# Kernel optimization log

Measured on AMD Instinct MI355X. Metric: run time of the kernel, lower is better.

## Reference

```python
import jax, jax.numpy as jnp
import numpy as np

N = 50000   # num_nodes
D = 128     # h_dim
R = 32      # num_rels * 2 (forward + inverse relations)
B = 8       # num_bases
E = 600000  # num_edges


def setup_inputs() -> dict:
    key = jax.random.key(0)
    ks = jax.random.split(key, 14)
    s = 1.0 / np.sqrt(D)
    return {
        "h_ids": jnp.arange(N, dtype=jnp.int32),
        "src": jax.random.randint(ks[0], (E,), 0, N),
        "dst": jax.random.randint(ks[1], (E,), 0, N),
        "etype": jax.random.randint(ks[2], (E,), 0, R),
        "norm": jax.random.uniform(ks[3], (E, 1), dtype=jnp.float32),
        "embedding": jax.random.normal(ks[4], (N, D), dtype=jnp.float32) * 0.05,
        "w_comp1": jax.random.normal(ks[5], (R, B), dtype=jnp.float32) * (1.0 / np.sqrt(B)),
        "bases1": jax.random.normal(ks[6], (B, D, D), dtype=jnp.float32) * s,
        "loop_w1": jax.random.normal(ks[7], (D, D), dtype=jnp.float32) * s,
        "bias1": jnp.zeros((D,), dtype=jnp.float32),
        "w_comp2": jax.random.normal(ks[8], (R, B), dtype=jnp.float32) * (1.0 / np.sqrt(B)),
        "bases2": jax.random.normal(ks[9], (B, D, D), dtype=jnp.float32) * s,
        "loop_w2": jax.random.normal(ks[10], (D, D), dtype=jnp.float32) * s,
        "bias2": jnp.zeros((D,), dtype=jnp.float32),
    }


def _rel_graph_conv(h, src, dst, etype, norm, w_comp, bases, loop_w, bias, act):
    # basis decomposition: W[r] = sum_b w_comp[r,b] * bases[b]
    W = jnp.einsum('rb,bio->rio', w_comp, bases)          # [R, D, D]
    # transform every node by every relation weight (dense GEMM)
    all_t = jnp.einsum('ni,rio->nro', h, W)               # [N, R, D]
    # per-edge gather of relation-specific transformed source features
    msg = all_t[src, etype] * norm                        # [E, D]
    # scatter-aggregate messages at destination nodes
    agg = jax.ops.segment_sum(msg, dst, num_segments=h.shape[0])  # [N, D]
    out = agg + h @ loop_w + bias                         # self-loop + bias
    return act(out) if act is not None else out


def reference(h_ids, src, dst, etype, norm, embedding,
              w_comp1, bases1, loop_w1, bias1,
              w_comp2, bases2, loop_w2, bias2):
    # EmbeddingLayer
    h = embedding[h_ids]                                  # [N, D]
    # hidden layer 0: relu activation (idx < num_hidden_layers-1)
    h = _rel_graph_conv(h, src, dst, etype, norm, w_comp1, bases1, loop_w1, bias1, jax.nn.relu)
    # hidden layer 1: no activation (last layer)
    h = _rel_graph_conv(h, src, dst, etype, norm, w_comp2, bases2, loop_w2, bias2, None)
    return h
```

## Files before the change

kernel.cpp:

```cpp
#include <hip/hip_runtime.h>

#define DD 128
#define NB 8
#define KTOT 1152

typedef unsigned int uint_t;
typedef __attribute__((ext_vector_type(8))) _Float16 half8v;
typedef __attribute__((ext_vector_type(2))) _Float16 half2v;
typedef __attribute__((ext_vector_type(4))) float f32x4;

static __device__ __forceinline__ void gld_lds16(const _Float16* g, _Float16* l)
{
  __builtin_amdgcn_global_load_lds(
      (const __attribute__((address_space(1))) void*)g,
      (__attribute__((address_space(3))) void*)l, 16, 0, 0);
}

static __device__ __forceinline__ half2v bc_h2(uint_t u)
{
  union { uint_t u; half2v h; } c; c.u = u; return c.h;
}

static __device__ __forceinline__ float fdot2(uint_t a, uint_t b, float acc)
{
#if __has_builtin(__builtin_amdgcn_fdot2)
  return __builtin_amdgcn_fdot2(bc_h2(a), bc_h2(b), acc, false);
#else
  half2v x = bc_h2(a), y = bc_h2(b);
  return acc + (float)x[0] * (float)y[0] + (float)x[1] * (float)y[1];
#endif
}

__global__ __launch_bounds__(256) void k_prep_w(
    const float* __restrict__ bases1, const float* __restrict__ loopw1,
    const float* __restrict__ bases2, const float* __restrict__ loopw2,
    _Float16* __restrict__ WcA)
{
  int i = blockIdx.x * 256 + threadIdx.x;
  if (i >= 2 * 36 * DD * 32) return;
  int layer = i / (36 * DD * 32);
  int rem   = i % (36 * DD * 32);
  int ks    = rem / (DD * 32);
  int rem2  = rem % (DD * 32);
  int feat  = rem2 / 32;
  int j     = rem2 % 32;
  int k     = ks * 32 + j;
  const float* basesL = layer ? bases2 : bases1;
  const float* loopwL = layer ? loopw2 : loopw1;
  float v;
  if (k < 1024) {
    int kk = k >> 3, b = k & 7;
    v = basesL[((size_t)b * DD + kk) * DD + feat];
  } else {
    v = loopwL[(size_t)(k - 1024) * DD + feat];
  }
  WcA[i] = (_Float16)v;
}

__global__ __launch_bounds__(256) void k_cast(
    const float* __restrict__ h, const int* __restrict__ ids,
    _Float16* __restrict__ hf, int N)
{
  int i = blockIdx.x * 256 + threadIdx.x;
  if (i >= N * (DD / 8)) return;
  int n  = i / (DD / 8);
  int k8 = (i % (DD / 8)) * 8;
  int row = ids ? ids[n] : n;
  const float* hp = h + (size_t)row * DD + k8;
  float4 v0 = *(const float4*)hp;
  float4 v1 = *(const float4*)(hp + 4);
  union { _Float16 e[8]; uint4 q; } p;
  p.e[0]=(_Float16)v0.x; p.e[1]=(_Float16)v0.y; p.e[2]=(_Float16)v0.z; p.e[3]=(_Float16)v0.w;
  p.e[4]=(_Float16)v1.x; p.e[5]=(_Float16)v1.y; p.e[6]=(_Float16)v1.z; p.e[7]=(_Float16)v1.w;
  *(uint4*)&hf[(size_t)n * DD + k8] = p.q;
}

__global__ __launch_bounds__(256) void k_zero(int* __restrict__ p, int n)
{
  int i = blockIdx.x * 256 + threadIdx.x;
  if (i < n) p[i] = 0;
}

__global__ __launch_bounds__(256) void k_hist(
    const int* __restrict__ dst, int* __restrict__ cnt, int E)
{
  int e = blockIdx.x * 256 + threadIdx.x;
  if (e < E) atomicAdd(&cnt[dst[e]], 1);
}

__global__ __launch_bounds__(256) void k_bsum(
    const int* __restrict__ cnt, int* __restrict__ bsum, int N)
{
  __shared__ int s[256];
  int i = blockIdx.x * 256 + threadIdx.x;
  s[threadIdx.x] = (i < N) ? ((cnt[i] + 1) & ~1) : 0;
  __syncthreads();
  for (int off = 128; off > 0; off >>= 1) {
    if (threadIdx.x < off) s[threadIdx.x] += s[threadIdx.x + off];
    __syncthreads();
  }
  if (threadIdx.x == 0) bsum[blockIdx.x] = s[0];
}

__global__ __launch_bounds__(256) void k_scanb(
    const int* __restrict__ bsum, int* __restrict__ boff, int nb)
{
  __shared__ int s[256];
  int t = threadIdx.x;
  int own = (t < nb) ? bsum[t] : 0;
  s[t] = own;
  __syncthreads();
  for (int off = 1; off < 256; off <<= 1) {
    int v = (t >= off) ? s[t - off] : 0;
    __syncthreads();
    s[t] += v;
    __syncthreads();
  }
  if (t < nb) boff[t] = s[t] - own;
}

__global__ __launch_bounds__(256) void k_scan3(
    const int* __restrict__ cnt, const int* __restrict__ boff,
    int* __restrict__ row_start, int N)
{
  __shared__ int s[256];
  int t = threadIdx.x;
  int i = blockIdx.x * 256 + t;
  int v = (i < N) ? ((cnt[i] + 1) & ~1) : 0;
  s[t] = v;
  __syncthreads();
  for (int off = 1; off < 256; off <<= 1) {
    int u = (t >= off) ? s[t - off] : 0;
    __syncthreads();
    s[t] += u;
    __syncthreads();
  }
  if (i < N) row_start[i] = boff[blockIdx.x] + s[t] - v;
}

__global__ __launch_bounds__(256) void k_pad(
    const int* __restrict__ rowst, const int* __restrict__ cnt,
    int* __restrict__ psrc, int N)
{
  int v = blockIdx.x * 256 + threadIdx.x;
  if (v < N && (cnt[v] & 1)) {
    int slot = rowst[v] + cnt[v];
    psrc[slot] = 0;
  }
}

__global__ __launch_bounds__(256) void k_place(
    const int* __restrict__ dst, const int* __restrict__ src,
    const int* __restrict__ etype, const float* __restrict__ norm,
    const int* __restrict__ row_start, int* __restrict__ cursor,
    int* __restrict__ psrc, int2* __restrict__ en, int E)
{
  int e = blockIdx.x * 256 + threadIdx.x;
  if (e < E) {
    int v = dst[e];
    int slot = row_start[v] + atomicAdd(&cursor[v], 1);
    psrc[slot] = src[e];
    en[slot] = make_int2(etype[e], __float_as_int(norm[e]));
  }
}

__global__ __launch_bounds__(256) void k_payload_pair(
    const int2* __restrict__ en,
    const float* __restrict__ wcomp1, const float* __restrict__ wcomp2,
    _Float16* __restrict__ c1, _Float16* __restrict__ c2, int npair)
{
  int i = blockIdx.x * 256 + threadIdx.x;
  if (i >= npair) return;
  int2 e0 = en[2 * i], e1 = en[2 * i + 1];
  float n0 = __int_as_float(e0.y), n1 = __int_as_float(e1.y);
  const float* w10 = wcomp1 + e0.x * NB;
  const float* w11 = wcomp1 + e1.x * NB;
  const float* w20 = wcomp2 + e0.x * NB;
  const float* w21 = wcomp2 + e1.x * NB;

  union { _Float16 h[16]; uint4 q[2]; } p;
  #pragma unroll
  for (int b = 0; b < NB; b++) {
    p.h[b * 2]     = (_Float16)(w10[b] * n0);
    p.h[b * 2 + 1] = (_Float16)(w11[b] * n1);
  }
  *(uint4*)&c1[(size_t)i * 16]     = p.q[0];
  *(uint4*)&c1[(size_t)i * 16 + 8] = p.q[1];
  #pragma unroll
  for (int b = 0; b < NB; b++) {
    p.h[b * 2]     = (_Float16)(w20[b] * n0);
    p.h[b * 2 + 1] = (_Float16)(w21[b] * n1);
  }
  *(uint4*)&c2[(size_t)i * 16]     = p.q[0];
  *(uint4*)&c2[(size_t)i * 16 + 8] = p.q[1];
}

__global__ __launch_bounds__(256) void k_agg(
    const int* __restrict__ rowst, const int* __restrict__ cnt,
    const int* __restrict__ psrc, const _Float16* __restrict__ cpair,
    const _Float16* __restrict__ hf,
    _Float16* __restrict__ agg, int N)
{
  int v = blockIdx.x * 4 + (threadIdx.x >> 6);
  if (v >= N) return;
  int lane = threadIdx.x & 63;
  const uint_t* hf32 = (const uint_t*)hf;
  const int beg = rowst[v];
  const int npairs = (cnt[v] + 1) >> 1;
  const uint_t* cp = (const uint_t*)cpair + (size_t)(beg >> 1) * 8;
  const int* ps = psrc + beg;

  float ax[NB] = {}, ay[NB] = {};
  int i = 0;
  for (; i + 2 <= npairs; i += 2) {
    int s0 = ps[2*i + 0], s1 = ps[2*i + 1];
    int s2 = ps[2*i + 2], s3 = ps[2*i + 3];
    uint_t u0 = hf32[(size_t)s0 * 64 + lane];
    uint_t u1 = hf32[(size_t)s1 * 64 + lane];
    uint_t u2 = hf32[(size_t)s2 * 64 + lane];
    uint_t u3 = hf32[(size_t)s3 * 64 + lane];
    uint_t lo01 = __builtin_amdgcn_perm(u0, u1, 0x01000504);
    uint_t hi01 = __builtin_amdgcn_perm(u0, u1, 0x03020706);
    uint_t lo23 = __builtin_amdgcn_perm(u2, u3, 0x01000504);
    uint_t hi23 = __builtin_amdgcn_perm(u2, u3, 0x03020706);
    #pragma unroll
    for (int b = 0; b < NB; b++) {
      uint_t ca = cp[(size_t)i * 8 + b];
      uint_t cb = cp[(size_t)(i + 1) * 8 + b];
      ax[b] = fdot2(ca, lo01, ax[b]);
      ay[b] = fdot2(ca, hi01, ay[b]);
      ax[b] = fdot2(cb, lo23, ax[b]);
      ay[b] = fdot2(cb, hi23, ay[b]);
    }
  }
  if (i < npairs) {
    int s0 = ps[2*i + 0], s1 = ps[2*i + 1];
    uint_t u0 = hf32[(size_t)s0 * 64 + lane];
    uint_t u1 = hf32[(size_t)s1 * 64 + lane];
    uint_t lo01 = __builtin_amdgcn_perm(u0, u1, 0x01000504);
    uint_t hi01 = __builtin_amdgcn_perm(u0, u1, 0x03020706);
    #pragma unroll
    for (int b = 0; b < NB; b++) {
      uint_t ca = cp[(size_t)i * 8 + b];
      ax[b] = fdot2(ca, lo01, ax[b]);
      ay[b] = fdot2(ca, hi01, ay[b]);
    }
  }

  union { _Float16 e[8]; uint4 q; } p0, p1;
  #pragma unroll
  for (int b = 0; b < NB; b++) { p0.e[b] = (_Float16)ax[b]; p1.e[b] = (_Float16)ay[b]; }
  uint4* dstp = (uint4*)&agg[(size_t)v * 1024 + lane * 16];
  dstp[0] = p0.q;
  dstp[1] = p1.q;
}

template <int LAYER>
__global__ __launch_bounds__(256) void k_mm(
    const _Float16* __restrict__ agg,
    const _Float16* __restrict__ hf,
    const _Float16* __restrict__ WcA,
    const float* __restrict__ bias,
    float* __restrict__ outf, _Float16* __restrict__ outh, int N)
{
  __shared__ _Float16 sB[2][2048];

  const int n0   = blockIdx.x * 32;
  const int wv   = threadIdx.x >> 6;
  const int lane = threadIdx.x & 63;
  const int l15  = lane & 15, l4 = lane >> 4;

  int nodeS = n0 + (lane & 31); if (nodeS >= N) nodeS = N - 1;
  const int ksl = 2 * wv + (lane >> 5);

  f32x4 acc[2][2];
  #pragma unroll
  for (int a = 0; a < 2; a++)
    #pragma unroll
    for (int b = 0; b < 2; b++) acc[a][b] = (f32x4)0.f;

  const int fbase = wv * 32 + l15;
  const int koff  = l4 * 8;

  auto STAGE = [&](int buf, int t) {
    const _Float16* g;
    if (t < 16) g = &agg[(size_t)nodeS * 1024 + t * 64 + ksl * 8];
    else        g = &hf [(size_t)nodeS * DD   + (t - 16) * 64 + ksl * 8];
    gld_lds16(g, &sB[buf][2 * wv * 256]);
  };

  auto COMPUTE = [&](int buf, int t) {
    #pragma unroll
    for (int sub = 0; sub < 2; sub++) {
      const int ks = 2 * t + sub;
      half8v af0 = *(const half8v*)&WcA[((size_t)ks * DD + fbase     ) * 32 + koff];
      half8v af1 = *(const half8v*)&WcA[((size_t)ks * DD + fbase + 16) * 32 + koff];
      half8v bf0 = *(const half8v*)&sB[buf][(sub * 4 + l4) * 256 + l15 * 8];
      half8v bf1 = *(const half8v*)&sB[buf][(sub * 4 + l4) * 256 + (16 + l15) * 8];
      acc[0][0] = __builtin_amdgcn_mfma_f32_16x16x32_f16(af0, bf0, acc[0][0], 0, 0, 0);
      acc[0][1] = __builtin_amdgcn_mfma_f32_16x16x32_f16(af0, bf1, acc[0][1], 0, 0, 0);
      acc[1][0] = __builtin_amdgcn_mfma_f32_16x16x32_f16(af1, bf0, acc[1][0], 0, 0, 0);
      acc[1][1] = __builtin_amdgcn_mfma_f32_16x16x32_f16(af1, bf1, acc[1][1], 0, 0, 0);
    }
  };

  STAGE(0, 0);
  int cur = 0;
  for (int t = 0; t < 18; t++) {
    if (t < 17) {
      STAGE(cur ^ 1, t + 1);
      asm volatile("s_waitcnt vmcnt(1)" ::: "memory");
    } else {
      asm volatile("s_waitcnt vmcnt(0)" ::: "memory");
    }
    __builtin_amdgcn_s_barrier();
    __builtin_amdgcn_sched_barrier(0);
    COMPUTE(cur, t);
    __builtin_amdgcn_sched_barrier(0);
    asm volatile("s_waitcnt lgkmcnt(0)" ::: "memory");
    __builtin_amdgcn_s_barrier();
    cur ^= 1;
  }

  #pragma unroll
  for (int mf = 0; mf < 2; mf++)
    #pragma unroll
    for (int nf = 0; nf < 2; nf++) {
      int n = n0 + nf * 16 + l15;
      if (n >= N) continue;
      int feat = wv * 32 + mf * 16 + l4 * 4;
      if (LAYER == 1) {
        union { _Float16 e[4]; uint2 q; } p;
        #pragma unroll
        for (int r = 0; r < 4; r++)
          p.e[r] = (_Float16)fmaxf(acc[mf][nf][r] + bias[feat + r], 0.f);
        *(uint2*)&outh[(size_t)n * DD + feat] = p.q;
      } else {
        float4 o;
        o.x = acc[mf][nf][0] + bias[feat + 0];
        o.y = acc[mf][nf][1] + bias[feat + 1];
        o.z = acc[mf][nf][2] + bias[feat + 2];
        o.w = acc[mf][nf][3] + bias[feat + 3];
        *(float4*)&outf[(size_t)n * DD + feat] = o;
      }
    }
}

extern "C" void kernel_launch(void* const* d_in, const int* in_sizes, int n_in,
                              void* d_out, int out_size, void* d_ws, size_t ws_size,
                              hipStream_t stream)
{
  const int*   h_ids     = (const int*)d_in[0];
  const int*   src       = (const int*)d_in[1];
  const int*   dst       = (const int*)d_in[2];
  const int*   etype     = (const int*)d_in[3];
  const float* norm      = (const float*)d_in[4];
  const float* embedding = (const float*)d_in[5];
  const float* w_comp1   = (const float*)d_in[6];
  const float* bases1    = (const float*)d_in[7];
  const float* loop_w1   = (const float*)d_in[8];
  const float* bias1     = (const float*)d_in[9];
  const float* w_comp2   = (const float*)d_in[10];
  const float* bases2    = (const float*)d_in[11];
  const float* loop_w2   = (const float*)d_in[12];
  const float* bias2     = (const float*)d_in[13];

  const int N = in_sizes[0];
  const int E = in_sizes[1];
  const int S = (E + N) & ~1;
  const int NPAIR = S >> 1;
  const int NBLK = (N + 255) / 256;

  char* base = (char*)d_ws;
  size_t off = 0;
  auto alloc = [&](size_t bytes) -> char* {
    char* p = base + off;
    off += (bytes + 255) & ~(size_t)255;
    return p;
  };
  _Float16* agg  = (_Float16*)alloc((size_t)N * 1024 * 2);
  _Float16* hfp  = (_Float16*)alloc((size_t)N * DD * 2);
  _Float16* h1h  = (_Float16*)alloc((size_t)N * DD * 2);
  _Float16* WcA  = (_Float16*)alloc((size_t)2 * 36 * DD * 32 * 2);
  int*      cnt    = (int*)   alloc((size_t)2 * N * 4);
  int*      cursor = cnt + N;
  int*      rowst  = (int*)   alloc((size_t)N * 4);
  int*      bsum   = (int*)   alloc(256 * 4);
  int*      boff   = (int*)   alloc(256 * 4);
  int*      psrc   = (int*)   alloc((size_t)S * 4);
  int2*     en     = (int2*)  alloc((size_t)S * 8);
  _Float16* c1     = (_Float16*)alloc((size_t)S * 8 * 2);
  _Float16* c2     = (_Float16*)alloc((size_t)S * 8 * 2);
  float*    out    = (float*)d_out;

  k_zero <<<(2 * N + 255) / 256, 256, 0, stream>>>(cnt, 2 * N);
  k_zero <<<(2 * S + 255) / 256, 256, 0, stream>>>((int*)en, 2 * S);
  k_hist <<<(E + 255) / 256, 256, 0, stream>>>(dst, cnt, E);
  k_bsum <<<NBLK, 256, 0, stream>>>(cnt, bsum, N);
  k_scanb<<<1, 256, 0, stream>>>(bsum, boff, NBLK);
  k_scan3<<<NBLK, 256, 0, stream>>>(cnt, boff, rowst, N);
  k_pad  <<<NBLK, 256, 0, stream>>>(rowst, cnt, psrc, N);
  k_place<<<(E + 255) / 256, 256, 0, stream>>>(dst, src, etype, norm,
                                               rowst, cursor, psrc, en, E);
  k_payload_pair<<<(NPAIR + 255) / 256, 256, 0, stream>>>(
      en, w_comp1, w_comp2, c1, c2, NPAIR);

  k_prep_w<<<(2 * 36 * DD * 32 + 255) / 256, 256, 0, stream>>>(bases1, loop_w1, bases2, loop_w2, WcA);

  dim3 gmm((N + 31) / 32);
  int gagg = (N + 3) / 4;

  k_cast<<<(N * (DD / 8) + 255) / 256, 256, 0, stream>>>(embedding, h_ids, hfp, N);
  k_agg<<<gagg, 256, 0, stream>>>(rowst, cnt, psrc, c1, hfp, agg, N);
  k_mm<1><<<gmm, 256, 0, stream>>>(agg, hfp, WcA, bias1, nullptr, h1h, N);

  k_agg<<<gagg, 256, 0, stream>>>(rowst, cnt, psrc, c2, h1h, agg, N);
  k_mm<2><<<gmm, 256, 0, stream>>>(agg, h1h, WcA + (size_t)36 * DD * 32, bias2, out, nullptr, N);
}
```

Baseline: 298.0 us.

## Stage whole node tile into LDS upfront instead of double-buffered pipeline

Replaces the two-buffer staged loop, which had a barrier pair every step, with a single burst of 18 async global-to-LDS loads covering all 1152 K values for the 32-node tile. One __syncthreads then gates a barrier-free MFMA loop over 36 k-slices. This removes per-iteration barriers and waits and issues all memory traffic at once. LDS use grows from 8 KB to 72 KB per block, which limits how many blocks fit per CU and so reduces latency hiding across blocks.

```diff
diff --git a/kernel.cpp b/kernel.cpp
--- a/kernel.cpp
+++ b/kernel.cpp
@@ -263,7 +263,7 @@
     const float* __restrict__ bias,
     float* __restrict__ outf, _Float16* __restrict__ outh, int N)
 {
-  __shared__ _Float16 sB[2][2048];
+  __shared__ _Float16 sB[18 * 2048];
 
   const int n0   = blockIdx.x * 32;
   const int wv   = threadIdx.x >> 6;
@@ -273,6 +273,17 @@
   int nodeS = n0 + (lane & 31); if (nodeS >= N) nodeS = N - 1;
   const int ksl = 2 * wv + (lane >> 5);
 
+  #pragma unroll
+  for (int t = 0; t < 16; t++)
+    gld_lds16(&agg[(size_t)nodeS * 1024 + t * 64 + ksl * 8],
+              &sB[t * 2048 + wv * 512]);
+  #pragma unroll
+  for (int t = 16; t < 18; t++)
+    gld_lds16(&hf[(size_t)nodeS * DD + (t - 16) * 64 + ksl * 8],
+              &sB[t * 2048 + wv * 512]);
+
+  __syncthreads();
+
   f32x4 acc[2][2];
   #pragma unroll
   for (int a = 0; a < 2; a++)
@@ -282,44 +293,17 @@
   const int fbase = wv * 32 + l15;
   const int koff  = l4 * 8;
 
-  auto STAGE = [&](int buf, int t) {
-    const _Float16* g;
-    if (t < 16) g = &agg[(size_t)nodeS * 1024 + t * 64 + ksl * 8];
-    else        g = &hf [(size_t)nodeS * DD   + (t - 16) * 64 + ksl * 8];
-    gld_lds16(g, &sB[buf][2 * wv * 256]);
-  };
-
-  auto COMPUTE = [&](int buf, int t) {
-    #pragma unroll
-    for (int sub = 0; sub < 2; sub++) {
-      const int ks = 2 * t + sub;
-      half8v af0 = *(const half8v*)&WcA[((size_t)ks * DD + fbase     ) * 32 + koff];
-      half8v af1 = *(const half8v*)&WcA[((size_t)ks * DD + fbase + 16) * 32 + koff];
-      half8v bf0 = *(const half8v*)&sB[buf][(sub * 4 + l4) * 256 + l15 * 8];
-      half8v bf1 = *(const half8v*)&sB[buf][(sub * 4 + l4) * 256 + (16 + l15) * 8];
-      acc[0][0] = __builtin_amdgcn_mfma_f32_16x16x32_f16(af0, bf0, acc[0][0], 0, 0, 0);
-      acc[0][1] = __builtin_amdgcn_mfma_f32_16x16x32_f16(af0, bf1, acc[0][1], 0, 0, 0);
-      acc[1][0] = __builtin_amdgcn_mfma_f32_16x16x32_f16(af1, bf0, acc[1][0], 0, 0, 0);
-      acc[1][1] = __builtin_amdgcn_mfma_f32_16x16x32_f16(af1, bf1, acc[1][1], 0, 0, 0);
-    }
-  };
-
-  STAGE(0, 0);
-  int cur = 0;
-  for (int t = 0; t < 18; t++) {
-    if (t < 17) {
-      STAGE(cur ^ 1, t + 1);
-      asm volatile("s_waitcnt vmcnt(1)" ::: "memory");
-    } else {
-      asm volatile("s_waitcnt vmcnt(0)" ::: "memory");
-    }
-    __builtin_amdgcn_s_barrier();
-    __builtin_amdgcn_sched_barrier(0);
-    COMPUTE(cur, t);
-    __builtin_amdgcn_sched_barrier(0);
-    asm volatile("s_waitcnt lgkmcnt(0)" ::: "memory");
-    __builtin_amdgcn_s_barrier();
-    cur ^= 1;
+  #pragma unroll 6
+  for (int ks = 0; ks < 36; ks++) {
+    half8v af0 = *(const half8v*)&WcA[((size_t)ks * DD + fbase     ) * 32 + koff];
+    half8v af1 = *(const half8v*)&WcA[((size_t)ks * DD + fbase + 16) * 32 + koff];
+    const _Float16* bb = &sB[(ks >> 1) * 2048 + ((ks & 1) * 4 + l4) * 256 + l15 * 8];
+    half8v bf0 = *(const half8v*)&bb[0];
+    half8v bf1 = *(const half8v*)&bb[128];
+    acc[0][0] = __builtin_amdgcn_mfma_f32_16x16x32_f16(af0, bf0, acc[0][0], 0, 0, 0);
+    acc[0][1] = __builtin_amdgcn_mfma_f32_16x16x32_f16(af0, bf1, acc[0][1], 0, 0, 0);
+    acc[1][0] = __builtin_amdgcn_mfma_f32_16x16x32_f16(af1, bf0, acc[1][0], 0, 0, 0);
+    acc[1][1] = __builtin_amdgcn_mfma_f32_16x16x32_f16(af1, bf1, acc[1][1], 0, 0, 0);
   }
 
   #pragma unroll
```

Measured after the change: 309.9 us. 1.04x slower.

## Widen k_mm node tile to 64 and stage weight tiles through LDS

Applied to the files above, without the earlier changes.

The GEMM kernel now processes 64 nodes per block instead of 32, so each weight fragment feeds four MFMA column tiles instead of two. The weight operand is now loaded into a double-buffered LDS tile with async global-to-LDS copies instead of being read from global memory inside the compute loop. The wait count is adjusted to match the larger number of in-flight loads per stage. This halves the grid size and cuts weight reloads per node. In exchange it uses more LDS and more accumulator registers, which may lower occupancy.

```diff
diff --git a/kernel.cpp b/kernel.cpp
--- a/kernel.cpp
+++ b/kernel.cpp
@@ -263,44 +263,58 @@
     const float* __restrict__ bias,
     float* __restrict__ outf, _Float16* __restrict__ outh, int N)
 {
-  __shared__ _Float16 sB[2][2048];
-
-  const int n0   = blockIdx.x * 32;
+  __shared__ _Float16 sA[2][8192];
+  __shared__ _Float16 sB[2][4096];
+
+  const int n0   = blockIdx.x * 64;
   const int wv   = threadIdx.x >> 6;
   const int lane = threadIdx.x & 63;
   const int l15  = lane & 15, l4 = lane >> 4;
 
-  int nodeS = n0 + (lane & 31); if (nodeS >= N) nodeS = N - 1;
-  const int ksl = 2 * wv + (lane >> 5);
-
-  f32x4 acc[2][2];
+  int nodeS = n0 + lane; if (nodeS >= N) nodeS = N - 1;
+
+  f32x4 acc[2][4];
   #pragma unroll
   for (int a = 0; a < 2; a++)
     #pragma unroll
-    for (int b = 0; b < 2; b++) acc[a][b] = (f32x4)0.f;
+    for (int b = 0; b < 4; b++) acc[a][b] = (f32x4)0.f;
 
   const int fbase = wv * 32 + l15;
   const int koff  = l4 * 8;
 
   auto STAGE = [&](int buf, int t) {
-    const _Float16* g;
-    if (t < 16) g = &agg[(size_t)nodeS * 1024 + t * 64 + ksl * 8];
-    else        g = &hf [(size_t)nodeS * DD   + (t - 16) * 64 + ksl * 8];
-    gld_lds16(g, &sB[buf][2 * wv * 256]);
+    #pragma unroll
+    for (int p = 0; p < 4; p++)
+      gld_lds16(&WcA[(size_t)t * 8192 + (p * 4 + wv) * 512 + lane * 8],
+                &sA[buf][(p * 4 + wv) * 512]);
+    if (t < 16) {
+      gld_lds16(&agg[(size_t)nodeS * 1024 + t * 64 + wv * 8],
+                &sB[buf][wv * 512]);
+      gld_lds16(&agg[(size_t)nodeS * 1024 + t * 64 + 32 + wv * 8],
+                &sB[buf][(wv + 4) * 512]);
+    } else {
+      gld_lds16(&hf[(size_t)nodeS * DD + (t - 16) * 64 + wv * 8],
+                &sB[buf][wv * 512]);
+      gld_lds16(&hf[(size_t)nodeS * DD + (t - 16) * 64 + 32 + wv * 8],
+                &sB[buf][(wv + 4) * 512]);
+    }
   };
 
-  auto COMPUTE = [&](int buf, int t) {
+  auto COMPUTE = [&](int buf) {
     #pragma unroll
     for (int sub = 0; sub < 2; sub++) {
-      const int ks = 2 * t + sub;
-      half8v af0 = *(const half8v*)&WcA[((size_t)ks * DD + fbase     ) * 32 + koff];
-      half8v af1 = *(const half8v*)&WcA[((size_t)ks * DD + fbase + 16) * 32 + koff];
-      half8v bf0 = *(const half8v*)&sB[buf][(sub * 4 + l4) * 256 + l15 * 8];
-      half8v bf1 = *(const half8v*)&sB[buf][(sub * 4 + l4) * 256 + (16 + l15) * 8];
-      acc[0][0] = __builtin_amdgcn_mfma_f32_16x16x32_f16(af0, bf0, acc[0][0], 0, 0, 0);
-      acc[0][1] = __builtin_amdgcn_mfma_f32_16x16x32_f16(af0, bf1, acc[0][1], 0, 0, 0);
-      acc[1][0] = __builtin_amdgcn_mfma_f32_16x16x32_f16(af1, bf0, acc[1][0], 0, 0, 0);
-      acc[1][1] = __builtin_amdgcn_mfma_f32_16x16x32_f16(af1, bf1, acc[1][1], 0, 0, 0);
+      half8v af[2], bfr[4];
+      #pragma unroll
+      for (int mf = 0; mf < 2; mf++)
+        af[mf] = *(const half8v*)&sA[buf][sub * 4096 + (fbase + mf * 16) * 32 + koff];
+      #pragma unroll
+      for (int nf = 0; nf < 4; nf++)
+        bfr[nf] = *(const half8v*)&sB[buf][(sub * 4 + l4) * 512 + (nf * 16 + l15) * 8];
+      #pragma unroll
+      for (int mf = 0; mf < 2; mf++)
+        #pragma unroll
+        for (int nf = 0; nf < 4; nf++)
+          acc[mf][nf] = __builtin_amdgcn_mfma_f32_16x16x32_f16(af[mf], bfr[nf], acc[mf][nf], 0, 0, 0);
     }
   };
 
@@ -309,13 +323,13 @@
   for (int t = 0; t < 18; t++) {
     if (t < 17) {
       STAGE(cur ^ 1, t + 1);
-      asm volatile("s_waitcnt vmcnt(1)" ::: "memory");
+      asm volatile("s_waitcnt vmcnt(6)" ::: "memory");
     } else {
       asm volatile("s_waitcnt vmcnt(0)" ::: "memory");
     }
     __builtin_amdgcn_s_barrier();
     __builtin_amdgcn_sched_barrier(0);
-    COMPUTE(cur, t);
+    COMPUTE(cur);
     __builtin_amdgcn_sched_barrier(0);
     asm volatile("s_waitcnt lgkmcnt(0)" ::: "memory");
     __builtin_amdgcn_s_barrier();
@@ -325,7 +339,7 @@
   #pragma unroll
   for (int mf = 0; mf < 2; mf++)
     #pragma unroll
-    for (int nf = 0; nf < 2; nf++) {
+    for (int nf = 0; nf < 4; nf++) {
       int n = n0 + nf * 16 + l15;
       if (n >= N) continue;
       int feat = wv * 32 + mf * 16 + l4 * 4;
@@ -407,7 +421,7 @@
 
   k_prep_w<<<(2 * 36 * DD * 32 + 255) / 256, 256, 0, stream>>>(bases1, loop_w1, bases2, loop_w2, WcA);
 
-  dim3 gmm((N + 31) / 32);
+  dim3 gmm((N + 63) / 64);
   int gagg = (N + 3) / 4;
 
   k_cast<<<(N * (DD / 8) + 255) / 256, 256, 0, stream>>>(embedding, h_ids, hfp, N);
```

Result: faster. 279.1 us (-6.4%).
